# Kernel tuning notes

Hardware: AMD Instinct MI355X
Metric: run time of the kernel (lower is better)

The kernel has to match this reference:

```python
import jax, jax.numpy as jnp
import numpy as np

B, T, C, H = 16, 2048, 1024, 64

def setup_inputs() -> dict:
    key = jax.random.key(0)
    kx, kq, kk, kv = jax.random.split(key, 4)
    s = 0.02
    return {
        "x": jax.random.normal(kx, (B, T, C), dtype=jnp.float32),
        "Wq": jax.random.normal(kq, (C, H), dtype=jnp.float32) * s,
        "Wk": jax.random.normal(kk, (C, H), dtype=jnp.float32) * s,
        "Wv": jax.random.normal(kv, (C, H), dtype=jnp.float32) * s,
    }

def reference(x, Wq, Wk, Wv):
    Bc, Tc, Cc = x.shape
    q = x @ Wq  # [B,T,H]
    k = x @ Wk  # [B,T,H]
    v = x @ Wv  # [B,T,H]
    # NOTE: original scales by n_embed^{-0.5} (C), not head_size^{-0.5}
    wei = jnp.einsum("bth,bsh->bts", q, k) * (Cc ** -0.5)  # [B,T,T]
    causal = jnp.tril(jnp.ones((Tc, Tc), dtype=bool))
    wei = jnp.where(causal, wei, -jnp.inf)
    wei = jax.nn.softmax(wei, axis=-1)
    # dropout is identity in eval mode
    out = jnp.einsum("bts,bsh->bth", wei, v)  # [B,T,H]
    return out
```

## Files before the change

kernel.cpp:

```cpp
#include <hip/hip_runtime.h>

typedef __attribute__((ext_vector_type(8))) short short8;
typedef __attribute__((ext_vector_type(4))) float float4v;

__device__ inline short f2bf(float f) {
    union { float f; unsigned int u; } c; c.f = f;
    unsigned int u = c.u;
    unsigned int r = (u + 0x7fffu + ((u >> 16) & 1u)) >> 16;
    return (short)r;
}

__device__ inline void gl2lds16(const short* g, short* l) {
    __builtin_amdgcn_global_load_lds(
        (const __attribute__((address_space(1))) unsigned int*)g,
        (__attribute__((address_space(3))) unsigned int*)l, 16, 0, 0);
}


__global__ __launch_bounds__(256) void wconv_kernel(
    const float* __restrict__ Wq, const float* __restrict__ Wk,
    const float* __restrict__ Wv, short* __restrict__ Wt_s)
{
    __shared__ short Ls[64 * 72];
    const int w  = blockIdx.x >> 4;
    const int c  = blockIdx.x & 15;
    const int k0 = c * 64;
    const float* W = (w == 0) ? Wq : (w == 1) ? Wk : Wv;
    const int tid = threadIdx.x;

#pragma unroll
    for (int i = 0; i < 4; i++) {
        int kk = (tid >> 4) + i * 16;
        int c4 = (tid & 15) * 4;
        float4 v = *(const float4*)&W[(size_t)(k0 + kk) * 64 + c4];
        Ls[kk * 72 + c4 + 0] = f2bf(v.x);
        Ls[kk * 72 + c4 + 1] = f2bf(v.y);
        Ls[kk * 72 + c4 + 2] = f2bf(v.z);
        Ls[kk * 72 + c4 + 3] = f2bf(v.w);
    }
    __syncthreads();
    const int n  = tid >> 2;
    const int k8 = (tid & 3) * 16;
    short8 o0, o1;
#pragma unroll
    for (int j = 0; j < 8; j++) o0[j] = Ls[(k8 + j) * 72 + n];
#pragma unroll
    for (int j = 0; j < 8; j++) o1[j] = Ls[(k8 + 8 + j) * 72 + n];
    const int gn = w * 64 + n;
    short* base = &Wt_s[((size_t)c * 192 + gn) * 64];
    int g0 = k8 >> 3;
    *(short8*)&base[((g0    ) ^ (gn & 7)) * 8] = o0;
    *(short8*)&base[((g0 + 1) ^ (gn & 7)) * 8] = o1;
}

__global__ __launch_bounds__(256) void qkv_kernel(
    const float* __restrict__ x, const short* __restrict__ Wt_s,
    short* __restrict__ qo, short* __restrict__ k_s, short* __restrict__ vT_t)
{
    __shared__ short As[32 * 72];
    __shared__ short Bs[192 * 64];

    const int tid  = threadIdx.x;
    const int wave = tid >> 6, lane = tid & 63;
    const int quad = lane >> 4, l16 = lane & 15;
    const int m0   = blockIdx.x * 32;

    float4v acc[2][3];
#pragma unroll
    for (int mf = 0; mf < 2; mf++)
#pragma unroll
        for (int nt = 0; nt < 3; nt++) acc[mf][nt] = (float4v)0.0f;

    const int arow = tid >> 3;
    const int acol = (tid & 7) * 8;
    const float* ap = &x[(size_t)(m0 + arow) * 1024 + acol];
    const int lofs = lane * 8;

    for (int kc = 0; kc < 1024; kc += 64) {
        __syncthreads();
        float4 x0 = *(const float4*)(ap + kc);
        float4 x1 = *(const float4*)(ap + kc + 4);
        short8 av;
        av[0]=f2bf(x0.x); av[1]=f2bf(x0.y); av[2]=f2bf(x0.z); av[3]=f2bf(x0.w);
        av[4]=f2bf(x1.x); av[5]=f2bf(x1.y); av[6]=f2bf(x1.z); av[7]=f2bf(x1.w);
        *(short8*)&As[arow * 72 + acol] = av;
        const short* gsrc = Wt_s + ((size_t)(kc >> 6) * 192 + wave * 48) * 64;
        short* ldst = &Bs[wave * 48 * 64];
#pragma unroll
        for (int i = 0; i < 6; i++)
            gl2lds16(gsrc + i * 512 + lofs, ldst + i * 512 + lofs);
        __syncthreads();
#pragma unroll
        for (int kc2 = 0; kc2 < 2; kc2++) {
            short8 a0 = *(const short8*)&As[(l16)      * 72 + kc2*32 + quad*8];
            short8 a1 = *(const short8*)&As[(16 + l16) * 72 + kc2*32 + quad*8];
#pragma unroll
            for (int nt = 0; nt < 3; nt++) {
                int brow = wave * 48 + nt * 16 + l16;
                int g = kc2 * 4 + quad;
                short8 bf = *(const short8*)&Bs[brow * 64 + (g ^ (brow & 7)) * 8];
                acc[0][nt] = __builtin_amdgcn_mfma_f32_16x16x32_bf16(a0, bf, acc[0][nt], 0, 0, 0);
                acc[1][nt] = __builtin_amdgcn_mfma_f32_16x16x32_bf16(a1, bf, acc[1][nt], 0, 0, 0);
            }
        }
    }
#pragma unroll
    for (int mf = 0; mf < 2; mf++) {
#pragma unroll
        for (int nt = 0; nt < 3; nt++) {
            int g = wave * 48 + nt * 16 + l16;
#pragma unroll
            for (int r = 0; r < 4; r++) {
                int row = m0 + mf * 16 + quad * 4 + r;
                short val = f2bf(acc[mf][nt][r]);
                if (g < 64) {
                    qo[(size_t)row * 64 + g] = val;
                } else if (g < 128) {
                    int h = g - 64;
                    k_s[(size_t)row * 64 + (((h >> 3) ^ (row & 7)) * 8 + (h & 7))] = val;
                } else {
                    int h = g - 128;
                    int bb = row >> 11, tt = row & 2047;
                    int tc = tt >> 6, tl = tt & 63;
                    vT_t[(((size_t)bb * 32 + tc) * 64 + h) * 64 +
                         (((tl >> 3) ^ (h & 7)) * 8 + (tl & 7))] = val;
                }
            }
        }
    }
}

#define SCALE_LOG2E 0.04508422132f

__global__ __launch_bounds__(128) void attn_kernel(
    const short* __restrict__ q, const short* __restrict__ k_s,
    const short* __restrict__ vT_t, float* __restrict__ out)
{
    __shared__ short Ks[64 * 64];
    __shared__ short Vs[64 * 64];
    __shared__ short Ps[32 * 72];

    const int tid  = threadIdx.x;
    const int wave = tid >> 6, lane = tid & 63;
    const int quad = lane >> 4, l16 = lane & 15;

    int b, qt;
    if (blockIdx.x < 512) { b = blockIdx.x >> 5; qt = 32 + (blockIdx.x & 31); }
    else { int t2 = blockIdx.x - 512; b = t2 >> 5; qt = 31 - (t2 & 31); }

    const short* kb = k_s  + (size_t)b * 2048 * 64;
    const short* vb = vT_t + (size_t)b * 32 * 64 * 64;

    const short* qrow = q + ((size_t)b * 2048 + qt*32 + wave*16 + l16) * 64;
    short8 qf0 = *(const short8*)&qrow[quad*8];
    short8 qf1 = *(const short8*)&qrow[32 + quad*8];

    float4v oacc[4];
#pragma unroll
    for (int t = 0; t < 4; t++) oacc[t] = (float4v)0.0f;
    float l_i[4] = {0.f, 0.f, 0.f, 0.f};

    const int tg   = qt*32 + wave*16 + quad*4;
    const int jmax = qt >> 1;
    const int lofs = lane * 8;

    for (int j = 0; j <= jmax; j++) {
        __syncthreads();
        const short* kg = kb + ((size_t)j * 64 + wave * 32) * 64;
        short* kl = &Ks[wave * 32 * 64];
#pragma unroll
        for (int i = 0; i < 4; i++)
            gl2lds16(kg + i * 512 + lofs, kl + i * 512 + lofs);
        const short* vg = vb + ((size_t)j * 64 + wave * 32) * 64;
        short* vl = &Vs[wave * 32 * 64];
#pragma unroll
        for (int i = 0; i < 4; i++)
            gl2lds16(vg + i * 512 + lofs, vl + i * 512 + lofs);
        __syncthreads();

        float4v sacc[4];
#pragma unroll
        for (int t = 0; t < 4; t++) sacc[t] = (float4v)0.0f;
#pragma unroll
        for (int t = 0; t < 4; t++) {
            int brow = t*16 + l16;
            short8 b0 = *(const short8*)&Ks[brow * 64 + ((    quad) ^ (brow & 7)) * 8];
            short8 b1 = *(const short8*)&Ks[brow * 64 + ((4 + quad) ^ (brow & 7)) * 8];
            sacc[t] = __builtin_amdgcn_mfma_f32_16x16x32_bf16(qf0, b0, sacc[t], 0, 0, 0);
            sacc[t] = __builtin_amdgcn_mfma_f32_16x16x32_bf16(qf1, b1, sacc[t], 0, 0, 0);
        }
        if (j == jmax) {
#pragma unroll
            for (int t = 0; t < 4; t++) {
                int sg = j*64 + t*16 + l16;
#pragma unroll
                for (int r = 0; r < 4; r++) {
                    float p = exp2f(sacc[t][r] * SCALE_LOG2E);
                    if (sg > tg + r) p = 0.0f;
                    sacc[t][r] = p;
                    l_i[r] += p;
                }
            }
        } else {
#pragma unroll
            for (int t = 0; t < 4; t++)
#pragma unroll
                for (int r = 0; r < 4; r++) {
                    float p = exp2f(sacc[t][r] * SCALE_LOG2E);
                    sacc[t][r] = p;
                    l_i[r] += p;
                }
        }
#pragma unroll
        for (int t = 0; t < 4; t++)
#pragma unroll
            for (int r = 0; r < 4; r++)
                Ps[(wave*16 + quad*4 + r) * 72 + t*16 + l16] = f2bf(sacc[t][r]);
#pragma unroll
        for (int kc = 0; kc < 2; kc++) {
            short8 af = *(const short8*)&Ps[(wave*16 + l16) * 72 + kc*32 + quad*8];
#pragma unroll
            for (int t = 0; t < 4; t++) {
                int drow = t*16 + l16;
                short8 bf = *(const short8*)&Vs[drow * 64 + ((kc*4 + quad) ^ (drow & 7)) * 8];
                oacc[t] = __builtin_amdgcn_mfma_f32_16x16x32_bf16(af, bf, oacc[t], 0, 0, 0);
            }
        }
    }
#pragma unroll
    for (int off = 1; off < 16; off <<= 1)
#pragma unroll
        for (int r = 0; r < 4; r++)
            l_i[r] += __shfl_xor(l_i[r], off, 64);
#pragma unroll
    for (int r = 0; r < 4; r++) {
        float inv = 1.0f / l_i[r];
        int row = qt*32 + wave*16 + quad*4 + r;
#pragma unroll
        for (int t = 0; t < 4; t++)
            out[((size_t)b * 2048 + row) * 64 + t*16 + l16] = oacc[t][r] * inv;
    }
}

extern "C" void kernel_launch(void* const* d_in, const int* in_sizes, int n_in,
                              void* d_out, int out_size, void* d_ws, size_t ws_size,
                              hipStream_t stream)
{
    const float* x  = (const float*)d_in[0];
    const float* Wq = (const float*)d_in[1];
    const float* Wk = (const float*)d_in[2];
    const float* Wv = (const float*)d_in[3];

    short* qw   = (short*)d_ws;
    short* ks   = qw + (size_t)32768 * 64;
    short* vTt  = ks + (size_t)32768 * 64;
    short* Wts  = vTt + (size_t)32768 * 64;
    float* out  = (float*)d_out;

    hipLaunchKernelGGL(wconv_kernel, dim3(48), dim3(256), 0, stream,
                       Wq, Wk, Wv, Wts);
    hipLaunchKernelGGL(qkv_kernel, dim3(1024), dim3(256), 0, stream,
                       x, Wts, qw, ks, vTt);
    hipLaunchKernelGGL(attn_kernel, dim3(1024), dim3(128), 0, stream,
                       qw, ks, vTt, out);
}
```

Before: 258.4 us.

## Double-buffer LDS loads and enlarge row tiles in QKV and attention kernels

The QKV projection now computes 64-row tiles per block instead of 32, so each weight chunk loaded into LDS serves more rows. The next x chunk and weight chunk are prefetched into a second LDS buffer while the current one is computed. The attention kernel now uses 4 waves covering 64 query rows with double-buffered K/V tiles, which cuts redundant K/V loads and overlaps the async global-to-LDS copies with MFMA work. The cost is more LDS and registers per block, which may lower occupancy, and the grid halves to 512 blocks, so there are fewer blocks to balance across CUs.

```diff
diff --git a/kernel.cpp b/kernel.cpp
--- a/kernel.cpp
+++ b/kernel.cpp
@@ -57,55 +57,94 @@
     const float* __restrict__ x, const short* __restrict__ Wt_s,
     short* __restrict__ qo, short* __restrict__ k_s, short* __restrict__ vT_t)
 {
-    __shared__ short As[32 * 72];
-    __shared__ short Bs[192 * 64];
+    __shared__ short As[2][64 * 72];
+    __shared__ short Bs[2][192 * 64];
 
     const int tid  = threadIdx.x;
     const int wave = tid >> 6, lane = tid & 63;
     const int quad = lane >> 4, l16 = lane & 15;
-    const int m0   = blockIdx.x * 32;
-
-    float4v acc[2][3];
-#pragma unroll
-    for (int mf = 0; mf < 2; mf++)
+    const int m0   = blockIdx.x * 64;
+
+    float4v acc[4][3];
+#pragma unroll
+    for (int mf = 0; mf < 4; mf++)
 #pragma unroll
         for (int nt = 0; nt < 3; nt++) acc[mf][nt] = (float4v)0.0f;
 
-    const int arow = tid >> 3;
-    const int acol = (tid & 7) * 8;
+    const int arow = tid >> 2;
+    const int acol = (tid & 3) * 16;
     const float* ap = &x[(size_t)(m0 + arow) * 1024 + acol];
     const int lofs = lane * 8;
 
-    for (int kc = 0; kc < 1024; kc += 64) {
-        __syncthreads();
-        float4 x0 = *(const float4*)(ap + kc);
-        float4 x1 = *(const float4*)(ap + kc + 4);
-        short8 av;
-        av[0]=f2bf(x0.x); av[1]=f2bf(x0.y); av[2]=f2bf(x0.z); av[3]=f2bf(x0.w);
-        av[4]=f2bf(x1.x); av[5]=f2bf(x1.y); av[6]=f2bf(x1.z); av[7]=f2bf(x1.w);
-        *(short8*)&As[arow * 72 + acol] = av;
-        const short* gsrc = Wt_s + ((size_t)(kc >> 6) * 192 + wave * 48) * 64;
-        short* ldst = &Bs[wave * 48 * 64];
+    {
+        float4 x0 = *(const float4*)(ap + 0);
+        float4 x1 = *(const float4*)(ap + 4);
+        float4 x2 = *(const float4*)(ap + 8);
+        float4 x3 = *(const float4*)(ap + 12);
+        const short* gsrc = Wt_s + ((size_t)wave * 48) * 64;
+        short* ldst = &Bs[0][wave * 48 * 64];
 #pragma unroll
         for (int i = 0; i < 6; i++)
             gl2lds16(gsrc + i * 512 + lofs, ldst + i * 512 + lofs);
-        __syncthreads();
+        short8 av0, av1;
+        av0[0]=f2bf(x0.x); av0[1]=f2bf(x0.y); av0[2]=f2bf(x0.z); av0[3]=f2bf(x0.w);
+        av0[4]=f2bf(x1.x); av0[5]=f2bf(x1.y); av0[6]=f2bf(x1.z); av0[7]=f2bf(x1.w);
+        av1[0]=f2bf(x2.x); av1[1]=f2bf(x2.y); av1[2]=f2bf(x2.z); av1[3]=f2bf(x2.w);
+        av1[4]=f2bf(x3.x); av1[5]=f2bf(x3.y); av1[6]=f2bf(x3.z); av1[7]=f2bf(x3.w);
+        *(short8*)&As[0][arow * 72 + acol]     = av0;
+        *(short8*)&As[0][arow * 72 + acol + 8] = av1;
+    }
+    __syncthreads();
+
+    int cur = 0;
+    for (int kc = 0; kc < 1024; kc += 64) {
+        const int nxt = cur ^ 1;
+        const bool pf = (kc + 64) < 1024;
+        float4 x0, x1, x2, x3;
+        if (pf) {
+            x0 = *(const float4*)(ap + kc + 64);
+            x1 = *(const float4*)(ap + kc + 68);
+            x2 = *(const float4*)(ap + kc + 72);
+            x3 = *(const float4*)(ap + kc + 76);
+            const short* gsrc = Wt_s + ((size_t)((kc >> 6) + 1) * 192 + wave * 48) * 64;
+            short* ldst = &Bs[nxt][wave * 48 * 64];
+#pragma unroll
+            for (int i = 0; i < 6; i++)
+                gl2lds16(gsrc + i * 512 + lofs, ldst + i * 512 + lofs);
+        }
+        const short* Asc = As[cur];
+        const short* Bsc = Bs[cur];
 #pragma unroll
         for (int kc2 = 0; kc2 < 2; kc2++) {
-            short8 a0 = *(const short8*)&As[(l16)      * 72 + kc2*32 + quad*8];
-            short8 a1 = *(const short8*)&As[(16 + l16) * 72 + kc2*32 + quad*8];
+            short8 a0 = *(const short8*)&Asc[(     l16) * 72 + kc2*32 + quad*8];
+            short8 a1 = *(const short8*)&Asc[(16 + l16) * 72 + kc2*32 + quad*8];
+            short8 a2 = *(const short8*)&Asc[(32 + l16) * 72 + kc2*32 + quad*8];
+            short8 a3 = *(const short8*)&Asc[(48 + l16) * 72 + kc2*32 + quad*8];
 #pragma unroll
             for (int nt = 0; nt < 3; nt++) {
                 int brow = wave * 48 + nt * 16 + l16;
                 int g = kc2 * 4 + quad;
-                short8 bf = *(const short8*)&Bs[brow * 64 + (g ^ (brow & 7)) * 8];
+                short8 bf = *(const short8*)&Bsc[brow * 64 + (g ^ (brow & 7)) * 8];
                 acc[0][nt] = __builtin_amdgcn_mfma_f32_16x16x32_bf16(a0, bf, acc[0][nt], 0, 0, 0);
                 acc[1][nt] = __builtin_amdgcn_mfma_f32_16x16x32_bf16(a1, bf, acc[1][nt], 0, 0, 0);
+                acc[2][nt] = __builtin_amdgcn_mfma_f32_16x16x32_bf16(a2, bf, acc[2][nt], 0, 0, 0);
+                acc[3][nt] = __builtin_amdgcn_mfma_f32_16x16x32_bf16(a3, bf, acc[3][nt], 0, 0, 0);
             }
         }
-    }
-#pragma unroll
-    for (int mf = 0; mf < 2; mf++) {
+        if (pf) {
+            short8 av0, av1;
+            av0[0]=f2bf(x0.x); av0[1]=f2bf(x0.y); av0[2]=f2bf(x0.z); av0[3]=f2bf(x0.w);
+            av0[4]=f2bf(x1.x); av0[5]=f2bf(x1.y); av0[6]=f2bf(x1.z); av0[7]=f2bf(x1.w);
+            av1[0]=f2bf(x2.x); av1[1]=f2bf(x2.y); av1[2]=f2bf(x2.z); av1[3]=f2bf(x2.w);
+            av1[4]=f2bf(x3.x); av1[5]=f2bf(x3.y); av1[6]=f2bf(x3.z); av1[7]=f2bf(x3.w);
+            *(short8*)&As[nxt][arow * 72 + acol]     = av0;
+            *(short8*)&As[nxt][arow * 72 + acol + 8] = av1;
+        }
+        __syncthreads();
+        cur = nxt;
+    }
+#pragma unroll
+    for (int mf = 0; mf < 4; mf++) {
 #pragma unroll
         for (int nt = 0; nt < 3; nt++) {
             int g = wave * 48 + nt * 16 + l16;
@@ -132,26 +171,26 @@
 
 #define SCALE_LOG2E 0.04508422132f
 
-__global__ __launch_bounds__(128) void attn_kernel(
+__global__ __launch_bounds__(256) void attn_kernel(
     const short* __restrict__ q, const short* __restrict__ k_s,
     const short* __restrict__ vT_t, float* __restrict__ out)
 {
-    __shared__ short Ks[64 * 64];
-    __shared__ short Vs[64 * 64];
-    __shared__ short Ps[32 * 72];
+    __shared__ short Ks[2][64 * 64];
+    __shared__ short Vs[2][64 * 64];
+    __shared__ short Ps[64 * 72];
 
     const int tid  = threadIdx.x;
     const int wave = tid >> 6, lane = tid & 63;
     const int quad = lane >> 4, l16 = lane & 15;
 
     int b, qt;
-    if (blockIdx.x < 512) { b = blockIdx.x >> 5; qt = 32 + (blockIdx.x & 31); }
-    else { int t2 = blockIdx.x - 512; b = t2 >> 5; qt = 31 - (t2 & 31); }
+    if (blockIdx.x < 256) { b = blockIdx.x >> 4; qt = 16 + (blockIdx.x & 15); }
+    else { int t2 = blockIdx.x - 256; b = t2 >> 4; qt = 15 - (t2 & 15); }
 
     const short* kb = k_s  + (size_t)b * 2048 * 64;
     const short* vb = vT_t + (size_t)b * 32 * 64 * 64;
 
-    const short* qrow = q + ((size_t)b * 2048 + qt*32 + wave*16 + l16) * 64;
+    const short* qrow = q + ((size_t)b * 2048 + qt*64 + wave*16 + l16) * 64;
     short8 qf0 = *(const short8*)&qrow[quad*8];
     short8 qf1 = *(const short8*)&qrow[32 + quad*8];
 
@@ -160,23 +199,37 @@
     for (int t = 0; t < 4; t++) oacc[t] = (float4v)0.0f;
     float l_i[4] = {0.f, 0.f, 0.f, 0.f};
 
-    const int tg   = qt*32 + wave*16 + quad*4;
-    const int jmax = qt >> 1;
+    const int tg   = qt*64 + wave*16 + quad*4;
+    const int jmax = qt;
     const int lofs = lane * 8;
 
+    {
+        const short* kg = kb + ((size_t)wave * 16) * 64;
+        short* kl = &Ks[0][wave * 16 * 64];
+        gl2lds16(kg +       lofs, kl +       lofs);
+        gl2lds16(kg + 512 + lofs, kl + 512 + lofs);
+        const short* vg = vb + ((size_t)wave * 16) * 64;
+        short* vl = &Vs[0][wave * 16 * 64];
+        gl2lds16(vg +       lofs, vl +       lofs);
+        gl2lds16(vg + 512 + lofs, vl + 512 + lofs);
+    }
+    __syncthreads();
+
+    int cur = 0;
     for (int j = 0; j <= jmax; j++) {
-        __syncthreads();
-        const short* kg = kb + ((size_t)j * 64 + wave * 32) * 64;
-        short* kl = &Ks[wave * 32 * 64];
-#pragma unroll
-        for (int i = 0; i < 4; i++)
-            gl2lds16(kg + i * 512 + lofs, kl + i * 512 + lofs);
-        const short* vg = vb + ((size_t)j * 64 + wave * 32) * 64;
-        short* vl = &Vs[wave * 32 * 64];
-#pragma unroll
-        for (int i = 0; i < 4; i++)
-            gl2lds16(vg + i * 512 + lofs, vl + i * 512 + lofs);
-        __syncthreads();
+        const int nxt = cur ^ 1;
+        if (j < jmax) {
+            const short* kg = kb + ((size_t)(j + 1) * 64 + wave * 16) * 64;
+            short* kl = &Ks[nxt][wave * 16 * 64];
+            gl2lds16(kg +       lofs, kl +       lofs);
+            gl2lds16(kg + 512 + lofs, kl + 512 + lofs);
+            const short* vg = vb + ((size_t)(j + 1) * 64 + wave * 16) * 64;
+            short* vl = &Vs[nxt][wave * 16 * 64];
+            gl2lds16(vg +       lofs, vl +       lofs);
+            gl2lds16(vg + 512 + lofs, vl + 512 + lofs);
+        }
+        const short* Ksc = Ks[cur];
+        const short* Vsc = Vs[cur];
 
         float4v sacc[4];
 #pragma unroll
@@ -184,8 +237,8 @@
 #pragma unroll
         for (int t = 0; t < 4; t++) {
             int brow = t*16 + l16;
-            short8 b0 = *(const short8*)&Ks[brow * 64 + ((    quad) ^ (brow & 7)) * 8];
-            short8 b1 = *(const short8*)&Ks[brow * 64 + ((4 + quad) ^ (brow & 7)) * 8];
+            short8 b0 = *(const short8*)&Ksc[brow * 64 + ((    quad) ^ (brow & 7)) * 8];
+            short8 b1 = *(const short8*)&Ksc[brow * 64 + ((4 + quad) ^ (brow & 7)) * 8];
             sacc[t] = __builtin_amdgcn_mfma_f32_16x16x32_bf16(qf0, b0, sacc[t], 0, 0, 0);
             sacc[t] = __builtin_amdgcn_mfma_f32_16x16x32_bf16(qf1, b1, sacc[t], 0, 0, 0);
         }
@@ -222,10 +275,12 @@
 #pragma unroll
             for (int t = 0; t < 4; t++) {
                 int drow = t*16 + l16;
-                short8 bf = *(const short8*)&Vs[drow * 64 + ((kc*4 + quad) ^ (drow & 7)) * 8];
+                short8 bf = *(const short8*)&Vsc[drow * 64 + ((kc*4 + quad) ^ (drow & 7)) * 8];
                 oacc[t] = __builtin_amdgcn_mfma_f32_16x16x32_bf16(af, bf, oacc[t], 0, 0, 0);
             }
         }
+        __syncthreads();
+        cur = nxt;
     }
 #pragma unroll
     for (int off = 1; off < 16; off <<= 1)
@@ -235,7 +290,7 @@
 #pragma unroll
     for (int r = 0; r < 4; r++) {
         float inv = 1.0f / l_i[r];
-        int row = qt*32 + wave*16 + quad*4 + r;
+        int row = qt*64 + wave*16 + quad*4 + r;
 #pragma unroll
         for (int t = 0; t < 4; t++)
             out[((size_t)b * 2048 + row) * 64 + t*16 + l16] = oacc[t][r] * inv;
@@ -259,8 +314,8 @@
 
     hipLaunchKernelGGL(wconv_kernel, dim3(48), dim3(256), 0, stream,
                        Wq, Wk, Wv, Wts);
-    hipLaunchKernelGGL(qkv_kernel, dim3(1024), dim3(256), 0, stream,
+    hipLaunchKernelGGL(qkv_kernel, dim3(512), dim3(256), 0, stream,
                        x, Wts, qw, ks, vTt);
-    hipLaunchKernelGGL(attn_kernel, dim3(1024), dim3(128), 0, stream,
+    hipLaunchKernelGGL(attn_kernel, dim3(512), dim3(256), 0, stream,
                        qw, ks, vTt, out);
 }
```

Result: faster. 251.5 us (-2.7%).
